# Kernel tuning notes

Hardware: AMD Instinct MI355X
Metric: run time of the kernel (lower is better)

## Reference

```python
import jax, jax.numpy as jnp
import numpy as np

N, E, CIN, HOPS, HID, COUT = 50000, 800000, 64, 3, 256, 64

def setup_inputs() -> dict:
    key = jax.random.key(0)
    ks = jax.random.split(key, 8)
    x = jax.random.normal(ks[0], (N, CIN), dtype=jnp.float32)
    edge_index = jax.random.randint(ks[1], (2, E), 0, N, dtype=jnp.int64)
    def lin(k, fan_in, fan_out):
        bound = 1.0 / np.sqrt(fan_in)
        return jax.random.uniform(k, (fan_in, fan_out), jnp.float32, -bound, bound)
    W0 = lin(ks[2], CIN * (HOPS + 1), HID)
    W1 = lin(ks[3], HID, HID)
    W2 = lin(ks[4], HID, COUT)
    b0 = jnp.zeros((HID,), jnp.float32)
    b1 = jnp.zeros((HID,), jnp.float32)
    b2 = jnp.zeros((COUT,), jnp.float32)
    return {"x": x, "edge_index": edge_index, "W0": W0, "b0": b0, "W1": W1, "b1": b1, "W2": W2, "b2": b2}

def reference(x, edge_index, W0, b0, W1, b1, W2, b2):
    row, col = edge_index[0], edge_index[1]
    n = x.shape[0]
    # degree of destination nodes (degree(col, N))
    d = jax.ops.segment_sum(jnp.ones_like(col, dtype=jnp.float32), col, num_segments=n)
    d_norm_in = 1.0 / jnp.sqrt(d[col])   # per-edge
    d_norm_out = 1.0 / jnp.sqrt(d[row])
    value = d_norm_in * d_norm_out
    value = jnp.where(jnp.isfinite(value), value, 0.0)  # nan_to_num
    def spmm(h):
        # adj has entries at (col[e], row[e]) -> out[i] = sum_{e: col[e]=i} value[e] * h[row[e]]
        return jax.ops.segment_sum(value[:, None] * h[row], col, num_segments=n)
    emb = [x]
    h = x
    for _ in range(HOPS):
        h = spmm(h)
        emb.append(h)
    z = jnp.concatenate(emb, axis=1)  # [N, CIN*(HOPS+1)]
    # eval mode: dropout is identity, use_bn=False
    z = jax.nn.relu(z @ W0 + b0)
    z = jax.nn.relu(z @ W1 + b1)
    return z @ W2 + b2
```

## Files before the change

### kernel.cpp

```cpp
#include <hip/hip_runtime.h>


#define ZW 256
#define NCH 64

typedef __attribute__((ext_vector_type(8))) __bf16 bf16x8;
typedef __attribute__((ext_vector_type(4))) float f32x4;

__device__ __forceinline__ unsigned f2bf(float f) {
    unsigned x = __float_as_uint(f);
    return (x + 0x7fffu + ((x >> 16) & 1u)) >> 16;
}
__device__ __forceinline__ unsigned pack_split(float v) {
    unsigned hb = f2bf(v);
    float hf = __uint_as_float(hb << 16);
    unsigned lb = f2bf(v - hf);
    return (hb << 16) | lb;
}
__device__ __forceinline__ float unpack_f(unsigned u) {
    return __uint_as_float(u & 0xffff0000u) + __uint_as_float(u << 16);
}

__device__ __forceinline__ void gload16(const void* g, void* l) {
    __builtin_amdgcn_global_load_lds(
        (const __attribute__((address_space(1))) unsigned*)g,
        (__attribute__((address_space(3))) unsigned*)l, 16, 0, 0);
}


__global__ void init_kernel(const float* __restrict__ x, unsigned* __restrict__ zp,
                            int* __restrict__ deg, int N) {
    int stride = gridDim.x * blockDim.x;
    int total4 = N * 16;
    for (int idx = blockIdx.x * blockDim.x + threadIdx.x; idx < total4; idx += stride) {
        int n = idx >> 4, c4 = idx & 15;
        float4 v = *reinterpret_cast<const float4*>(x + (size_t)n * NCH + c4 * 4);
        uint4 o;
        o.x = pack_split(v.x); o.y = pack_split(v.y);
        o.z = pack_split(v.z); o.w = pack_split(v.w);
        *reinterpret_cast<uint4*>(zp + (size_t)n * ZW + c4 * 4) = o;
    }
    for (int idx = blockIdx.x * blockDim.x + threadIdx.x; idx < N; idx += stride)
        deg[idx] = 0;
}

__global__ void degree_kernel(const int* __restrict__ col, int* __restrict__ deg,
                              int E, int N) {
    int slice = blockIdx.x & 7;
    int g = blockIdx.x >> 3;
    int G = gridDim.x >> 3;
    int sliceN = (N + 7) >> 3;
    int lo = slice * sliceN;
    int hi = lo + sliceN; if (hi > N) hi = N;
    int stride = G * blockDim.x;
    for (int e = g * blockDim.x + threadIdx.x; e < E; e += stride) {
        int c = col[e];
        if (c >= lo && c < hi) atomicAdd(&deg[c], 1);
    }
}

__global__ __launch_bounds__(1024) void scan_part_kernel(const int* __restrict__ deg,
                                                         int* __restrict__ off,
                                                         int* __restrict__ bsum, int N) {
    __shared__ int smem[1024];
    int tid = threadIdx.x;
    int i = blockIdx.x * 1024 + tid;
    int v = (i < N) ? deg[i] : 0;
    smem[tid] = v;
    __syncthreads();
    for (int o = 1; o < 1024; o <<= 1) {
        int t = (tid >= o) ? smem[tid - o] : 0;
        __syncthreads();
        smem[tid] += t;
        __syncthreads();
    }
    if (i < N) off[i] = smem[tid] - v;
    if (tid == 1023) bsum[blockIdx.x] = smem[1023];
}

__global__ void scan_tops_kernel(const int* __restrict__ bsum, int* __restrict__ btot, int nb) {
    int lane = threadIdx.x;
    int v = (lane < nb) ? bsum[lane] : 0;
    int incl = v;
    for (int o = 1; o < 64; o <<= 1) {
        int t = __shfl_up(incl, o);
        if (lane >= o) incl += t;
    }
    if (lane < nb) btot[lane] = incl - v;
    if (lane == 63) btot[nb] = incl;
}

__global__ __launch_bounds__(1024) void scan_add_kernel(int* __restrict__ off,
                                                        int* __restrict__ cur,
                                                        const int* __restrict__ btot,
                                                        int N, int nb) {
    int i = blockIdx.x * 1024 + threadIdx.x;
    if (i < N) {
        int o = off[i] + btot[blockIdx.x];
        off[i] = o;
        cur[i] = o;
    }
    if (i == 0) off[N] = btot[nb];
}

__global__ void scatter_kernel(const int* __restrict__ row, const int* __restrict__ col,
                               const int* __restrict__ deg, int* __restrict__ cursor,
                               int2* __restrict__ meta, int E, int N) {
    int slice = blockIdx.x & 7;
    int g = blockIdx.x >> 3;
    int G = gridDim.x >> 3;
    int sliceN = (N + 7) >> 3;
    int lo = slice * sliceN;
    int hi = lo + sliceN; if (hi > N) hi = N;
    int stride = G * blockDim.x;
    for (int e = g * blockDim.x + threadIdx.x; e < E; e += stride) {
        int c = col[e];
        if (c >= lo && c < hi) {
            int r = row[e];
            int dc = deg[c];
            int dr = deg[r];
            float v = 0.0f;
            if (dc > 0 && dr > 0) v = rsqrtf((float)dc * (float)dr);
            int pos = atomicAdd(&cursor[c], 1);
            meta[pos] = make_int2(r, __float_as_int(v));
        }
    }
}

__global__ void spmm_csr_kernel(const int* __restrict__ offsets, const int2* __restrict__ meta,
                                const unsigned* __restrict__ zin, unsigned* __restrict__ zout,
                                int N) {
    int lane = threadIdx.x & 63;
    int wave = (blockIdx.x * blockDim.x + threadIdx.x) >> 6;
    if (wave >= N) return;
    int start = offsets[wave];
    int end   = offsets[wave + 1];
    float acc = 0.0f;
    int j = start;
    for (; j + 4 <= end; j += 4) {
        int2 m0 = meta[j];
        int2 m1 = meta[j + 1];
        int2 m2 = meta[j + 2];
        int2 m3 = meta[j + 3];
        float h0 = unpack_f(zin[(size_t)m0.x * ZW + lane]);
        float h1 = unpack_f(zin[(size_t)m1.x * ZW + lane]);
        float h2 = unpack_f(zin[(size_t)m2.x * ZW + lane]);
        float h3 = unpack_f(zin[(size_t)m3.x * ZW + lane]);
        acc = fmaf(__int_as_float(m0.y), h0, acc);
        acc = fmaf(__int_as_float(m1.y), h1, acc);
        acc = fmaf(__int_as_float(m2.y), h2, acc);
        acc = fmaf(__int_as_float(m3.y), h3, acc);
    }
    for (; j + 2 <= end; j += 2) {
        int2 m0 = meta[j];
        int2 m1 = meta[j + 1];
        float h0 = unpack_f(zin[(size_t)m0.x * ZW + lane]);
        float h1 = unpack_f(zin[(size_t)m1.x * ZW + lane]);
        acc = fmaf(__int_as_float(m0.y), h0, acc);
        acc = fmaf(__int_as_float(m1.y), h1, acc);
    }
    if (j < end) {
        int2 m0 = meta[j];
        acc = fmaf(__int_as_float(m0.y), unpack_f(zin[(size_t)m0.x * ZW + lane]), acc);
    }
    zout[(size_t)wave * ZW + lane] = pack_split(acc);
}

__global__ void prep_w_kernel(const float* __restrict__ W0, const float* __restrict__ W1,
                              const float* __restrict__ W2, unsigned short* __restrict__ ws) {
    int idx = blockIdx.x * blockDim.x + threadIdx.x;
    if (idx >= 65536) return;
    int n = idx >> 8, k = idx & 255;
    unsigned p0 = pack_split(W0[(size_t)k * 256 + n]);
    ws[idx]          = (unsigned short)(p0 >> 16);
    ws[65536 + idx]  = (unsigned short)(p0 & 0xffff);
    unsigned p1 = pack_split(W1[(size_t)k * 256 + n]);
    ws[131072 + idx] = (unsigned short)(p1 >> 16);
    ws[196608 + idx] = (unsigned short)(p1 & 0xffff);
    if (idx < 16384) {
        int n2 = idx >> 8, k2 = idx & 255;
        unsigned p2 = pack_split(W2[(size_t)k2 * 64 + n2]);
        ws[262144 + idx] = (unsigned short)(p2 >> 16);
        ws[278528 + idx] = (unsigned short)(p2 & 0xffff);
    }
}

__global__ __launch_bounds__(256, 3) void gemm256_kernel(
        const unsigned* __restrict__ Ap, const unsigned short* __restrict__ Wh,
        const unsigned short* __restrict__ Wl, const float* __restrict__ bias,
        unsigned* __restrict__ Cp, int M) {
    __shared__ unsigned Apl[2 * 128 * 32];

    int tid = threadIdx.x;
    int lane = tid & 63;
    int wid = tid >> 6;
    int wr = wid >> 1, wc = wid & 1;
    int bm = blockIdx.x * 128;
    int bn = blockIdx.y * 128;
    int l15 = lane & 15, kg = lane >> 4;

    f32x4 acc[4][4] = {};

    auto STAGE = [&](int buf, int k0) {
        unsigned* Ab = Apl + buf * (128 * 32);
#pragma unroll
        for (int i = 0; i < 4; ++i) {
            int s = (wid * 4 + i) * 64 + lane;
            int r = s >> 3, cp = s & 7;
            int cl = cp ^ (r & 7);
            int grow = bm + r; if (grow >= M) grow = M - 1;
            gload16(Ap + (size_t)grow * 256 + k0 + cl * 4, Ab + (wid * 4 + i) * 256);
        }
    };

    auto COMPUTE = [&](int buf, int k0) {
        const unsigned* Ab = Apl + buf * (128 * 32);
        bf16x8 bh[4], bl[4];
#pragma unroll
        for (int n4 = 0; n4 < 4; ++n4) {
            int nn = wc * 64 + n4 * 16 + l15;
            size_t go = (size_t)(bn + nn) * 256 + k0 + kg * 8;
            bh[n4] = *reinterpret_cast<const bf16x8*>(Wh + go);
            bl[n4] = *reinterpret_cast<const bf16x8*>(Wl + go);
        }
#pragma unroll
        for (int m = 0; m < 4; ++m) {
            int r = wr * 64 + m * 16 + l15;
            int c0 = (2 * kg) ^ (r & 7);
            int c1 = (2 * kg + 1) ^ (r & 7);
            uint4 q0 = *reinterpret_cast<const uint4*>(&Ab[r * 32 + c0 * 4]);
            uint4 q1 = *reinterpret_cast<const uint4*>(&Ab[r * 32 + c1 * 4]);
            union { bf16x8 v; unsigned short s[8]; } ah, al;
            ah.s[0] = (unsigned short)(q0.x >> 16); al.s[0] = (unsigned short)q0.x;
            ah.s[1] = (unsigned short)(q0.y >> 16); al.s[1] = (unsigned short)q0.y;
            ah.s[2] = (unsigned short)(q0.z >> 16); al.s[2] = (unsigned short)q0.z;
            ah.s[3] = (unsigned short)(q0.w >> 16); al.s[3] = (unsigned short)q0.w;
            ah.s[4] = (unsigned short)(q1.x >> 16); al.s[4] = (unsigned short)q1.x;
            ah.s[5] = (unsigned short)(q1.y >> 16); al.s[5] = (unsigned short)q1.y;
            ah.s[6] = (unsigned short)(q1.z >> 16); al.s[6] = (unsigned short)q1.z;
            ah.s[7] = (unsigned short)(q1.w >> 16); al.s[7] = (unsigned short)q1.w;
#pragma unroll
            for (int n4 = 0; n4 < 4; ++n4) {
                acc[m][n4] = __builtin_amdgcn_mfma_f32_16x16x32_bf16(ah.v, bh[n4], acc[m][n4], 0, 0, 0);
                acc[m][n4] = __builtin_amdgcn_mfma_f32_16x16x32_bf16(ah.v, bl[n4], acc[m][n4], 0, 0, 0);
                acc[m][n4] = __builtin_amdgcn_mfma_f32_16x16x32_bf16(al.v, bh[n4], acc[m][n4], 0, 0, 0);
            }
        }
    };

    STAGE(0, 0);
#pragma unroll
    for (int t = 0; t < 8; ++t) {
        if (t < 7) {
            STAGE((t + 1) & 1, (t + 1) * 32);
            asm volatile("s_waitcnt vmcnt(4)" ::: "memory");
        } else {
            asm volatile("s_waitcnt vmcnt(0)" ::: "memory");
        }
        __builtin_amdgcn_s_barrier();
        COMPUTE(t & 1, t * 32);
        __builtin_amdgcn_s_barrier();
        __builtin_amdgcn_sched_barrier(0);
    }

#pragma unroll
    for (int n4 = 0; n4 < 4; ++n4) {
        int col = bn + wc * 64 + n4 * 16 + l15;
        float bv = bias[col];
#pragma unroll
        for (int m = 0; m < 4; ++m) {
#pragma unroll
            for (int rr = 0; rr < 4; ++rr) {
                int row = bm + wr * 64 + m * 16 + kg * 4 + rr;
                if (row < M) {
                    float v = fmaxf(acc[m][n4][rr] + bv, 0.0f);
                    Cp[(size_t)row * 256 + col] = pack_split(v);
                }
            }
        }
    }
}

__global__ __launch_bounds__(256, 3) void gemm64_kernel(
        const unsigned* __restrict__ Ap, const unsigned short* __restrict__ Wh,
        const unsigned short* __restrict__ Wl, const float* __restrict__ bias,
        float* __restrict__ out, int M) {
    __shared__ unsigned Apl[2 * 128 * 32];

    int tid = threadIdx.x;
    int lane = tid & 63;
    int wid = tid >> 6;
    int bm = blockIdx.x * 128;
    int l15 = lane & 15, kg = lane >> 4;

    f32x4 acc[2][4] = {};

    auto STAGE = [&](int buf, int k0) {
        unsigned* Ab = Apl + buf * (128 * 32);
#pragma unroll
        for (int i = 0; i < 4; ++i) {
            int s = (wid * 4 + i) * 64 + lane;
            int r = s >> 3, cp = s & 7;
            int cl = cp ^ (r & 7);
            int grow = bm + r; if (grow >= M) grow = M - 1;
            gload16(Ap + (size_t)grow * 256 + k0 + cl * 4, Ab + (wid * 4 + i) * 256);
        }
    };

    auto COMPUTE = [&](int buf, int k0) {
        const unsigned* Ab = Apl + buf * (128 * 32);
        bf16x8 bh[4], bl[4];
#pragma unroll
        for (int n4 = 0; n4 < 4; ++n4) {
            int nn = n4 * 16 + l15;
            size_t go = (size_t)nn * 256 + k0 + kg * 8;
            bh[n4] = *reinterpret_cast<const bf16x8*>(Wh + go);
            bl[n4] = *reinterpret_cast<const bf16x8*>(Wl + go);
        }
#pragma unroll
        for (int m = 0; m < 2; ++m) {
            int r = wid * 32 + m * 16 + l15;
            int c0 = (2 * kg) ^ (r & 7);
            int c1 = (2 * kg + 1) ^ (r & 7);
            uint4 q0 = *reinterpret_cast<const uint4*>(&Ab[r * 32 + c0 * 4]);
            uint4 q1 = *reinterpret_cast<const uint4*>(&Ab[r * 32 + c1 * 4]);
            union { bf16x8 v; unsigned short s[8]; } ah, al;
            ah.s[0] = (unsigned short)(q0.x >> 16); al.s[0] = (unsigned short)q0.x;
            ah.s[1] = (unsigned short)(q0.y >> 16); al.s[1] = (unsigned short)q0.y;
            ah.s[2] = (unsigned short)(q0.z >> 16); al.s[2] = (unsigned short)q0.z;
            ah.s[3] = (unsigned short)(q0.w >> 16); al.s[3] = (unsigned short)q0.w;
            ah.s[4] = (unsigned short)(q1.x >> 16); al.s[4] = (unsigned short)q1.x;
            ah.s[5] = (unsigned short)(q1.y >> 16); al.s[5] = (unsigned short)q1.y;
            ah.s[6] = (unsigned short)(q1.z >> 16); al.s[6] = (unsigned short)q1.z;
            ah.s[7] = (unsigned short)(q1.w >> 16); al.s[7] = (unsigned short)q1.w;
#pragma unroll
            for (int n4 = 0; n4 < 4; ++n4) {
                acc[m][n4] = __builtin_amdgcn_mfma_f32_16x16x32_bf16(ah.v, bh[n4], acc[m][n4], 0, 0, 0);
                acc[m][n4] = __builtin_amdgcn_mfma_f32_16x16x32_bf16(ah.v, bl[n4], acc[m][n4], 0, 0, 0);
                acc[m][n4] = __builtin_amdgcn_mfma_f32_16x16x32_bf16(al.v, bh[n4], acc[m][n4], 0, 0, 0);
            }
        }
    };

    STAGE(0, 0);
#pragma unroll
    for (int t = 0; t < 8; ++t) {
        if (t < 7) {
            STAGE((t + 1) & 1, (t + 1) * 32);
            asm volatile("s_waitcnt vmcnt(4)" ::: "memory");
        } else {
            asm volatile("s_waitcnt vmcnt(0)" ::: "memory");
        }
        __builtin_amdgcn_s_barrier();
        COMPUTE(t & 1, t * 32);
        __builtin_amdgcn_s_barrier();
        __builtin_amdgcn_sched_barrier(0);
    }

#pragma unroll
    for (int n4 = 0; n4 < 4; ++n4) {
        int col = n4 * 16 + l15;
        float bv = bias[col];
#pragma unroll
        for (int m = 0; m < 2; ++m) {
#pragma unroll
            for (int rr = 0; rr < 4; ++rr) {
                int row = bm + wid * 32 + m * 16 + kg * 4 + rr;
                if (row < M) out[(size_t)row * 64 + col] = acc[m][n4][rr] + bv;
            }
        }
    }
}

extern "C" void kernel_launch(void* const* d_in, const int* in_sizes, int n_in,
                              void* d_out, int out_size, void* d_ws, size_t ws_size,
                              hipStream_t stream) {
    const float* x  = (const float*)d_in[0];
    const int* ei   = (const int*)d_in[1];
    const float* W0 = (const float*)d_in[2];
    const float* b0 = (const float*)d_in[3];
    const float* W1 = (const float*)d_in[4];
    const float* b1 = (const float*)d_in[5];
    const float* W2 = (const float*)d_in[6];
    const float* b2 = (const float*)d_in[7];
    float* out = (float*)d_out;

    const int N = in_sizes[0] / NCH;
    const int E = in_sizes[1] / 2;
    const int* row = ei;
    const int* col = ei + E;

    unsigned* zp = (unsigned*)d_ws;
    unsigned* hp = zp + (size_t)N * ZW;
    unsigned short* wsp = (unsigned short*)(hp + (size_t)N * ZW);
    int* deg  = (int*)(wsp + 294912);
    int* off  = deg + N;
    int* cur  = off + N + 1;
    int* bsum = cur + N;
    int* btot = bsum + 64;
    int2* meta = (int2*)hp;

    const int TB = 256;
    const int NB = (N + 1023) / 1024;

    prep_w_kernel<<<256, TB, 0, stream>>>(W0, W1, W2, wsp);
    init_kernel<<<2048, TB, 0, stream>>>(x, zp, deg, N);
    degree_kernel<<<1024, TB, 0, stream>>>(col, deg, E, N);
    scan_part_kernel<<<NB, 1024, 0, stream>>>(deg, off, bsum, N);
    scan_tops_kernel<<<1, 64, 0, stream>>>(bsum, btot, NB);
    scan_add_kernel<<<NB, 1024, 0, stream>>>(off, cur, btot, N, NB);
    scatter_kernel<<<1024, TB, 0, stream>>>(row, col, deg, cur, meta, E, N);

    int spmm_blocks = (N * 64 + TB - 1) / TB;
    for (int hop = 1; hop <= 3; ++hop) {
        const unsigned* zin = zp + (hop - 1) * NCH;
        unsigned* zout      = zp + hop * NCH;
        spmm_csr_kernel<<<spmm_blocks, TB, 0, stream>>>(off, meta, zin, zout, N);
    }

    int gblocks = (N + 127) / 128;
    dim3 g256(gblocks, 2);
    gemm256_kernel<<<g256, TB, 0, stream>>>(zp, wsp,          wsp + 65536,  b0, hp, N);
    gemm256_kernel<<<g256, TB, 0, stream>>>(hp, wsp + 131072, wsp + 196608, b1, zp, N);
    gemm64_kernel<<<gblocks, TB, 0, stream>>>(zp, wsp + 262144, wsp + 278528, b2, out, N);
}
```

Measured before the change: 417.9 us.

## Fuse three MLP GEMM layers into one kernel keeping hidden activations in LDS

Replaces the three separate GEMM launches with a single kernel that processes 64-row tiles through all three layers. Each hidden activation tile is kept in a swizzled 64KB LDS buffer instead of being written to and read back from global memory. This removes the global round-trips of the 50000x256 intermediates and two kernel launches. In exchange the tile is smaller, LDS use per block is higher, occupancy drops to two blocks per CU, and the layer-1/2 loops read weights directly from global memory with no prefetch pipeline.

```diff
diff --git a/kernel.cpp b/kernel.cpp
--- a/kernel.cpp
+++ b/kernel.cpp
@@ -25,6 +25,18 @@
     __builtin_amdgcn_global_load_lds(
         (const __attribute__((address_space(1))) unsigned*)g,
         (__attribute__((address_space(3))) unsigned*)l, 16, 0, 0);
+}
+
+union bfu { bf16x8 v; unsigned short s[8]; };
+__device__ __forceinline__ void unpack8(uint4 q0, uint4 q1, bfu& ah, bfu& al) {
+    ah.s[0] = (unsigned short)(q0.x >> 16); al.s[0] = (unsigned short)q0.x;
+    ah.s[1] = (unsigned short)(q0.y >> 16); al.s[1] = (unsigned short)q0.y;
+    ah.s[2] = (unsigned short)(q0.z >> 16); al.s[2] = (unsigned short)q0.z;
+    ah.s[3] = (unsigned short)(q0.w >> 16); al.s[3] = (unsigned short)q0.w;
+    ah.s[4] = (unsigned short)(q1.x >> 16); al.s[4] = (unsigned short)q1.x;
+    ah.s[5] = (unsigned short)(q1.y >> 16); al.s[5] = (unsigned short)q1.y;
+    ah.s[6] = (unsigned short)(q1.z >> 16); al.s[6] = (unsigned short)q1.z;
+    ah.s[7] = (unsigned short)(q1.w >> 16); al.s[7] = (unsigned short)q1.w;
 }
 
 
@@ -185,60 +197,59 @@
     }
 }
 
-__global__ __launch_bounds__(256, 3) void gemm256_kernel(
-        const unsigned* __restrict__ Ap, const unsigned short* __restrict__ Wh,
-        const unsigned short* __restrict__ Wl, const float* __restrict__ bias,
-        unsigned* __restrict__ Cp, int M) {
-    __shared__ unsigned Apl[2 * 128 * 32];
+__global__ __launch_bounds__(256, 2) void mlp_fused_kernel(
+        const unsigned* __restrict__ Ap, const unsigned short* __restrict__ wsp,
+        const float* __restrict__ b0, const float* __restrict__ b1,
+        const float* __restrict__ b2, float* __restrict__ out, int M) {
+    __shared__ unsigned Ast[2 * 64 * 32];
+    __shared__ unsigned Hs[64 * 256];
+
+    const unsigned short* W0h = wsp;
+    const unsigned short* W0l = wsp + 65536;
+    const unsigned short* W1h = wsp + 131072;
+    const unsigned short* W1l = wsp + 196608;
+    const unsigned short* W2h = wsp + 262144;
+    const unsigned short* W2l = wsp + 278528;
 
     int tid = threadIdx.x;
     int lane = tid & 63;
     int wid = tid >> 6;
-    int wr = wid >> 1, wc = wid & 1;
-    int bm = blockIdx.x * 128;
-    int bn = blockIdx.y * 128;
+    int bm = blockIdx.x * 64;
     int l15 = lane & 15, kg = lane >> 4;
 
     f32x4 acc[4][4] = {};
 
     auto STAGE = [&](int buf, int k0) {
-        unsigned* Ab = Apl + buf * (128 * 32);
-#pragma unroll
-        for (int i = 0; i < 4; ++i) {
-            int s = (wid * 4 + i) * 64 + lane;
+        unsigned* Ab = Ast + buf * 2048;
+#pragma unroll
+        for (int q = 0; q < 2; ++q) {
+            int s = (wid * 2 + q) * 64 + lane;
             int r = s >> 3, cp = s & 7;
             int cl = cp ^ (r & 7);
             int grow = bm + r; if (grow >= M) grow = M - 1;
-            gload16(Ap + (size_t)grow * 256 + k0 + cl * 4, Ab + (wid * 4 + i) * 256);
+            gload16(Ap + (size_t)grow * 256 + k0 + cl * 4, Ab + (wid * 2 + q) * 256);
         }
     };
 
-    auto COMPUTE = [&](int buf, int k0) {
-        const unsigned* Ab = Apl + buf * (128 * 32);
+    auto COMPUTE0 = [&](int buf, int k0) {
+        const unsigned* Ab = Ast + buf * 2048;
         bf16x8 bh[4], bl[4];
 #pragma unroll
         for (int n4 = 0; n4 < 4; ++n4) {
-            int nn = wc * 64 + n4 * 16 + l15;
-            size_t go = (size_t)(bn + nn) * 256 + k0 + kg * 8;
-            bh[n4] = *reinterpret_cast<const bf16x8*>(Wh + go);
-            bl[n4] = *reinterpret_cast<const bf16x8*>(Wl + go);
+            int nn = wid * 64 + n4 * 16 + l15;
+            size_t go = (size_t)nn * 256 + k0 + kg * 8;
+            bh[n4] = *reinterpret_cast<const bf16x8*>(W0h + go);
+            bl[n4] = *reinterpret_cast<const bf16x8*>(W0l + go);
         }
 #pragma unroll
         for (int m = 0; m < 4; ++m) {
-            int r = wr * 64 + m * 16 + l15;
+            int r = m * 16 + l15;
             int c0 = (2 * kg) ^ (r & 7);
             int c1 = (2 * kg + 1) ^ (r & 7);
             uint4 q0 = *reinterpret_cast<const uint4*>(&Ab[r * 32 + c0 * 4]);
             uint4 q1 = *reinterpret_cast<const uint4*>(&Ab[r * 32 + c1 * 4]);
-            union { bf16x8 v; unsigned short s[8]; } ah, al;
-            ah.s[0] = (unsigned short)(q0.x >> 16); al.s[0] = (unsigned short)q0.x;
-            ah.s[1] = (unsigned short)(q0.y >> 16); al.s[1] = (unsigned short)q0.y;
-            ah.s[2] = (unsigned short)(q0.z >> 16); al.s[2] = (unsigned short)q0.z;
-            ah.s[3] = (unsigned short)(q0.w >> 16); al.s[3] = (unsigned short)q0.w;
-            ah.s[4] = (unsigned short)(q1.x >> 16); al.s[4] = (unsigned short)q1.x;
-            ah.s[5] = (unsigned short)(q1.y >> 16); al.s[5] = (unsigned short)q1.y;
-            ah.s[6] = (unsigned short)(q1.z >> 16); al.s[6] = (unsigned short)q1.z;
-            ah.s[7] = (unsigned short)(q1.w >> 16); al.s[7] = (unsigned short)q1.w;
+            bfu ah, al;
+            unpack8(q0, q1, ah, al);
 #pragma unroll
             for (int n4 = 0; n4 < 4; ++n4) {
                 acc[m][n4] = __builtin_amdgcn_mfma_f32_16x16x32_bf16(ah.v, bh[n4], acc[m][n4], 0, 0, 0);
@@ -253,86 +264,52 @@
     for (int t = 0; t < 8; ++t) {
         if (t < 7) {
             STAGE((t + 1) & 1, (t + 1) * 32);
-            asm volatile("s_waitcnt vmcnt(4)" ::: "memory");
+            asm volatile("s_waitcnt vmcnt(2)" ::: "memory");
         } else {
             asm volatile("s_waitcnt vmcnt(0)" ::: "memory");
         }
         __builtin_amdgcn_s_barrier();
-        COMPUTE(t & 1, t * 32);
+        COMPUTE0(t & 1, t * 32);
         __builtin_amdgcn_s_barrier();
         __builtin_amdgcn_sched_barrier(0);
     }
 
+    auto hwrite = [&](int r, int c, float v) {
+        int j = (c >> 2) ^ (r & 7);
+        Hs[r * 256 + j * 4 + (c & 3)] = pack_split(v);
+    };
 #pragma unroll
     for (int n4 = 0; n4 < 4; ++n4) {
-        int col = bn + wc * 64 + n4 * 16 + l15;
-        float bv = bias[col];
+        int c = wid * 64 + n4 * 16 + l15;
+        float bv = b0[c];
+#pragma unroll
+        for (int m = 0; m < 4; ++m)
+#pragma unroll
+            for (int rr = 0; rr < 4; ++rr) {
+                int r = m * 16 + kg * 4 + rr;
+                hwrite(r, c, fmaxf(acc[m][n4][rr] + bv, 0.0f));
+                acc[m][n4][rr] = 0.0f;
+            }
+    }
+    __syncthreads();
+
+    for (int k0 = 0; k0 < 256; k0 += 32) {
+        bf16x8 bh[4], bl[4];
+#pragma unroll
+        for (int n4 = 0; n4 < 4; ++n4) {
+            int nn = wid * 64 + n4 * 16 + l15;
+            size_t go = (size_t)nn * 256 + k0 + kg * 8;
+            bh[n4] = *reinterpret_cast<const bf16x8*>(W1h + go);
+            bl[n4] = *reinterpret_cast<const bf16x8*>(W1l + go);
+        }
 #pragma unroll
         for (int m = 0; m < 4; ++m) {
-#pragma unroll
-            for (int rr = 0; rr < 4; ++rr) {
-                int row = bm + wr * 64 + m * 16 + kg * 4 + rr;
-                if (row < M) {
-                    float v = fmaxf(acc[m][n4][rr] + bv, 0.0f);
-                    Cp[(size_t)row * 256 + col] = pack_split(v);
-                }
-            }
-        }
-    }
-}
-
-__global__ __launch_bounds__(256, 3) void gemm64_kernel(
-        const unsigned* __restrict__ Ap, const unsigned short* __restrict__ Wh,
-        const unsigned short* __restrict__ Wl, const float* __restrict__ bias,
-        float* __restrict__ out, int M) {
-    __shared__ unsigned Apl[2 * 128 * 32];
-
-    int tid = threadIdx.x;
-    int lane = tid & 63;
-    int wid = tid >> 6;
-    int bm = blockIdx.x * 128;
-    int l15 = lane & 15, kg = lane >> 4;
-
-    f32x4 acc[2][4] = {};
-
-    auto STAGE = [&](int buf, int k0) {
-        unsigned* Ab = Apl + buf * (128 * 32);
-#pragma unroll
-        for (int i = 0; i < 4; ++i) {
-            int s = (wid * 4 + i) * 64 + lane;
-            int r = s >> 3, cp = s & 7;
-            int cl = cp ^ (r & 7);
-            int grow = bm + r; if (grow >= M) grow = M - 1;
-            gload16(Ap + (size_t)grow * 256 + k0 + cl * 4, Ab + (wid * 4 + i) * 256);
-        }
-    };
-
-    auto COMPUTE = [&](int buf, int k0) {
-        const unsigned* Ab = Apl + buf * (128 * 32);
-        bf16x8 bh[4], bl[4];
-#pragma unroll
-        for (int n4 = 0; n4 < 4; ++n4) {
-            int nn = n4 * 16 + l15;
-            size_t go = (size_t)nn * 256 + k0 + kg * 8;
-            bh[n4] = *reinterpret_cast<const bf16x8*>(Wh + go);
-            bl[n4] = *reinterpret_cast<const bf16x8*>(Wl + go);
-        }
-#pragma unroll
-        for (int m = 0; m < 2; ++m) {
-            int r = wid * 32 + m * 16 + l15;
-            int c0 = (2 * kg) ^ (r & 7);
-            int c1 = (2 * kg + 1) ^ (r & 7);
-            uint4 q0 = *reinterpret_cast<const uint4*>(&Ab[r * 32 + c0 * 4]);
-            uint4 q1 = *reinterpret_cast<const uint4*>(&Ab[r * 32 + c1 * 4]);
-            union { bf16x8 v; unsigned short s[8]; } ah, al;
-            ah.s[0] = (unsigned short)(q0.x >> 16); al.s[0] = (unsigned short)q0.x;
-            ah.s[1] = (unsigned short)(q0.y >> 16); al.s[1] = (unsigned short)q0.y;
-            ah.s[2] = (unsigned short)(q0.z >> 16); al.s[2] = (unsigned short)q0.z;
-            ah.s[3] = (unsigned short)(q0.w >> 16); al.s[3] = (unsigned short)q0.w;
-            ah.s[4] = (unsigned short)(q1.x >> 16); al.s[4] = (unsigned short)q1.x;
-            ah.s[5] = (unsigned short)(q1.y >> 16); al.s[5] = (unsigned short)q1.y;
-            ah.s[6] = (unsigned short)(q1.z >> 16); al.s[6] = (unsigned short)q1.z;
-            ah.s[7] = (unsigned short)(q1.w >> 16); al.s[7] = (unsigned short)q1.w;
+            int r = m * 16 + l15;
+            int jb = (k0 >> 2) + 2 * kg;
+            uint4 q0 = *reinterpret_cast<const uint4*>(&Hs[r * 256 + (jb ^ (r & 7)) * 4]);
+            uint4 q1 = *reinterpret_cast<const uint4*>(&Hs[r * 256 + ((jb + 1) ^ (r & 7)) * 4]);
+            bfu ah, al;
+            unpack8(q0, q1, ah, al);
 #pragma unroll
             for (int n4 = 0; n4 < 4; ++n4) {
                 acc[m][n4] = __builtin_amdgcn_mfma_f32_16x16x32_bf16(ah.v, bh[n4], acc[m][n4], 0, 0, 0);
@@ -340,35 +317,51 @@
                 acc[m][n4] = __builtin_amdgcn_mfma_f32_16x16x32_bf16(al.v, bh[n4], acc[m][n4], 0, 0, 0);
             }
         }
-    };
-
-    STAGE(0, 0);
-#pragma unroll
-    for (int t = 0; t < 8; ++t) {
-        if (t < 7) {
-            STAGE((t + 1) & 1, (t + 1) * 32);
-            asm volatile("s_waitcnt vmcnt(4)" ::: "memory");
-        } else {
-            asm volatile("s_waitcnt vmcnt(0)" ::: "memory");
-        }
-        __builtin_amdgcn_s_barrier();
-        COMPUTE(t & 1, t * 32);
-        __builtin_amdgcn_s_barrier();
-        __builtin_amdgcn_sched_barrier(0);
-    }
-
+    }
+    __syncthreads();
 #pragma unroll
     for (int n4 = 0; n4 < 4; ++n4) {
-        int col = n4 * 16 + l15;
-        float bv = bias[col];
-#pragma unroll
-        for (int m = 0; m < 2; ++m) {
+        int c = wid * 64 + n4 * 16 + l15;
+        float bv = b1[c];
+#pragma unroll
+        for (int m = 0; m < 4; ++m)
 #pragma unroll
             for (int rr = 0; rr < 4; ++rr) {
-                int row = bm + wid * 32 + m * 16 + kg * 4 + rr;
-                if (row < M) out[(size_t)row * 64 + col] = acc[m][n4][rr] + bv;
+                int r = m * 16 + kg * 4 + rr;
+                hwrite(r, c, fmaxf(acc[m][n4][rr] + bv, 0.0f));
             }
-        }
+    }
+    __syncthreads();
+
+    f32x4 acc2[4] = {};
+    for (int k0 = 0; k0 < 256; k0 += 32) {
+        int nn = wid * 16 + l15;
+        size_t go = (size_t)nn * 256 + k0 + kg * 8;
+        bf16x8 bh2 = *reinterpret_cast<const bf16x8*>(W2h + go);
+        bf16x8 bl2 = *reinterpret_cast<const bf16x8*>(W2l + go);
+#pragma unroll
+        for (int m = 0; m < 4; ++m) {
+            int r = m * 16 + l15;
+            int jb = (k0 >> 2) + 2 * kg;
+            uint4 q0 = *reinterpret_cast<const uint4*>(&Hs[r * 256 + (jb ^ (r & 7)) * 4]);
+            uint4 q1 = *reinterpret_cast<const uint4*>(&Hs[r * 256 + ((jb + 1) ^ (r & 7)) * 4]);
+            bfu ah, al;
+            unpack8(q0, q1, ah, al);
+            acc2[m] = __builtin_amdgcn_mfma_f32_16x16x32_bf16(ah.v, bh2, acc2[m], 0, 0, 0);
+            acc2[m] = __builtin_amdgcn_mfma_f32_16x16x32_bf16(ah.v, bl2, acc2[m], 0, 0, 0);
+            acc2[m] = __builtin_amdgcn_mfma_f32_16x16x32_bf16(al.v, bh2, acc2[m], 0, 0, 0);
+        }
+    }
+    {
+        int c = wid * 16 + l15;
+        float bv = b2[c];
+#pragma unroll
+        for (int m = 0; m < 4; ++m)
+#pragma unroll
+            for (int rr = 0; rr < 4; ++rr) {
+                int row = bm + m * 16 + kg * 4 + rr;
+                if (row < M) out[(size_t)row * 64 + c] = acc2[m][rr] + bv;
+            }
     }
 }
 
@@ -418,9 +411,6 @@
         spmm_csr_kernel<<<spmm_blocks, TB, 0, stream>>>(off, meta, zin, zout, N);
     }
 
-    int gblocks = (N + 127) / 128;
-    dim3 g256(gblocks, 2);
-    gemm256_kernel<<<g256, TB, 0, stream>>>(zp, wsp,          wsp + 65536,  b0, hp, N);
-    gemm256_kernel<<<g256, TB, 0, stream>>>(hp, wsp + 131072, wsp + 196608, b1, zp, N);
-    gemm64_kernel<<<gblocks, TB, 0, stream>>>(zp, wsp + 262144, wsp + 278528, b2, out, N);
-}
+    int mblocks = (N + 63) / 64;
+    mlp_fused_kernel<<<mblocks, TB, 0, stream>>>(zp, wsp, b0, b1, b2, out, N);
+}
```

Measured after the change: 350.3 us. 1.19x faster.
